# Performance work log

Hardware: AMD Instinct MI355X
Metric: run time of the kernel (lower is better)

The kernel has to match this reference:

```python
import jax, jax.numpy as jnp
import numpy as np

# Fixed hyperparameters from init_kwargs
KH, KW = 3, 3
GRID_SIZE = 5
SPLINE_ORDER = 3
GRID_RANGE = (-1.0, 1.0)


def _make_grid():
    # grid buffer: arange(-k, grid_size + k + 1) * h + grid_range[0], shape (G + 2k + 1,) = (12,)
    h = (GRID_RANGE[1] - GRID_RANGE[0]) / GRID_SIZE
    return (jnp.arange(-SPLINE_ORDER, GRID_SIZE + SPLINE_ORDER + 1, dtype=jnp.float32) * h
            + GRID_RANGE[0])


def _unfold(x):
    # torch.nn.Unfold with kernel (3,3), stride 1, pad 0, dilation 1.
    # Returns (N, C*KH*KW) with channel-major ordering (c, i, j), matching torch.
    B, C, H, W = x.shape
    Ho, Wo = H - KH + 1, W - KW + 1
    cols = [x[:, :, i:i + Ho, j:j + Wo] for i in range(KH) for j in range(KW)]
    p = jnp.stack(cols, axis=2)                    # (B, C, KH*KW, Ho, Wo)
    p = p.reshape(B, C * KH * KW, Ho * Wo)         # (B, in_features, L)
    p = p.transpose(0, 2, 1).reshape(-1, C * KH * KW)  # (B*L, in_features)
    return p, Ho, Wo


def _b_splines(x, grid):
    # x: (N, in_features); grid: (G + 2k + 1,) uniform, shared across features.
    # Returns (N, in_features, G + k) B-spline basis via Cox-de Boor recursion.
    x = x[..., None]  # (N, in, 1)
    bases = ((x >= grid[:-1]) & (x < grid[1:])).astype(x.dtype)  # (N, in, G+2k)
    for k in range(1, SPLINE_ORDER + 1):
        left = (x - grid[: -(k + 1)]) / (grid[k:-1] - grid[: -(k + 1)])
        right = (grid[k + 1:] - x) / (grid[k + 1:] - grid[1:-k])
        bases = left * bases[..., :-1] + right * bases[..., 1:]
    return bases  # (N, in, G + k)


def setup_inputs() -> dict:
    key = jax.random.key(0)
    k1, k2, k3, k4 = jax.random.split(key, 4)
    in_features = 32 * KH * KW  # 288
    out_features = 64
    n_coef = GRID_SIZE + SPLINE_ORDER  # 8
    x = jax.random.normal(k1, (16, 32, 64, 64), dtype=jnp.float32)
    base_weight = jax.random.normal(k2, (out_features, in_features), dtype=jnp.float32) * (1.0 / np.sqrt(in_features))
    spline_weight = jax.random.normal(k3, (out_features, in_features, n_coef), dtype=jnp.float32) * 0.1
    spline_scaler = jax.random.normal(k4, (out_features, in_features), dtype=jnp.float32) * (1.0 / np.sqrt(in_features))
    return {"x": x, "base_weight": base_weight, "spline_weight": spline_weight,
            "spline_scaler": spline_scaler}


def reference(x, base_weight, spline_weight, spline_scaler):
    B = x.shape[0]
    out_features = base_weight.shape[0]
    grid = _make_grid()

    patches, Ho, Wo = _unfold(x)                              # (N, in_features)
    N, in_features = patches.shape

    # KANLinear forward
    base_out = jnp.matmul(jax.nn.relu(patches), base_weight.T)  # (N, out)
    bases = _b_splines(patches, grid)                           # (N, in, G+k)
    scaled_w = spline_weight * spline_scaler[..., None]         # (out, in, G+k)
    spline_out = jnp.matmul(bases.reshape(N, -1), scaled_w.reshape(out_features, -1).T)
    out = base_out + spline_out                                 # (N, out)

    out = out.reshape(B, Ho, Wo, out_features).transpose(0, 3, 1, 2)  # (B, C_out, Ho, Wo)
    return out
```

## Files before the change

### kernel.cpp

```cpp
#include <hip/hip_runtime.h>
#include <stdint.h>

typedef _Float16 half8  __attribute__((ext_vector_type(8)));
typedef float    f32x4  __attribute__((ext_vector_type(4)));
typedef float    f32x16 __attribute__((ext_vector_type(16)));
typedef uint32_t u32x4  __attribute__((ext_vector_type(4)));

#define FIN  288
#define NOUT 64
#define LPB  3844
#define NBF  20736
#define NBAS (16*64*16*64*2)
#define NXR  (16*64*2*64*2)
#define PADS 16

#define SCL  200
#define LDSL (31*SCL + 2*64 + 64 + 8)


__device__ inline half8 bspline8(float xv) {
  float u = fmaf(xv, 2.5f, 5.5f);
  float fi = floorf(u);
  int i = (int)fi;
  float t = u - fi, s = 1.0f - t;
  float t2 = t * t, t3 = t2 * t;
  float s2 = s * s, s3 = s2 * s;
  float w3 = t3 * 0.16666667f;
  float w0 = s3 * 0.16666667f;
  float w1 = fmaf(0.5f, t3, -t2) + 0.66666667f;
  float w2 = fmaf(0.5f, s3, -s2) + 0.66666667f;
  uint32_t u01 = __builtin_bit_cast(uint32_t, __builtin_amdgcn_cvt_pkrtz(w0, w1));
  uint32_t u23 = __builtin_bit_cast(uint32_t, __builtin_amdgcn_cvt_pkrtz(w2, w3));
  uint64_t V = (uint64_t)u01 | ((uint64_t)u23 << 32);
  uint32_t vl = (uint32_t)(V << 16);
  u32x4 fr;
#pragma unroll
  for (int q = 0; q < 4; ++q) {
    int d = i - 2 * q;
    uint32_t rr = (uint32_t)(V >> ((48 - 16 * d) & 63));
    fr[q] = ((uint32_t)d <= 3u) ? rr : ((d == 4) ? vl : 0u);
  }
  return __builtin_bit_cast(half8, fr);
}

__global__ __launch_bounds__(256) void prep_all(const float* __restrict__ x,
                                                const float* __restrict__ bw,
                                                const float* __restrict__ sw,
                                                const float* __restrict__ sc,
                                                half8* __restrict__ ws) {
  int bid = blockIdx.x;
  if (bid < 2048) {
    int t = bid * 256 + threadIdx.x;
    int w4   = t & 15;
    int idx  = t >> 4;
    int half = idx & 1;
    int u    = (idx >> 1) & 15;
    int bh   = idx >> 5;
    int c    = u * 2 + half;
    const float4 v = *(const float4*)(x + (bh >> 6) * 131072 + c * 4096 +
                                      (bh & 63) * 64 + w4 * 4);
    half8* dst = ws + NBF + ((size_t)(bh * 16 + u) * 64 + w4 * 4) * 2 + half;
    dst[0] = bspline8(v.x);
    dst[2] = bspline8(v.y);
    dst[4] = bspline8(v.z);
    dst[6] = bspline8(v.w);
  } else if (bid < 3072) {
    int t = (bid - 2048) * 256 + threadIdx.x;
    int half = t & 1;
    int w    = (t >> 1) & 63;
    int u    = (t >> 7) & 1;
    int bh   = t >> 8;
    const float* xp = x + (bh >> 6) * 131072 + (u * 16 + half * 8) * 4096 +
                      (bh & 63) * 64 + w;
    half8 v;
#pragma unroll
    for (int j = 0; j < 8; ++j) v[j] = (_Float16)fmaxf(xp[j * 4096], 0.0f);
    ws[NBF + NBAS + ((size_t)(bh * 2 + u) * 64 + w) * 2 + half] = v;
  } else {
    int t = (bid - 3072) * 256 + threadIdx.x;
    half8 v;
    int dst;
    if (t < NOUT * FIN) {
      int o = t / FIN;
      int f = t - o * FIN;
      float scale = sc[t];
      const float* p = sw + t * 8;
#pragma unroll
      for (int j = 0; j < 8; ++j) v[j] = (_Float16)(p[j] * scale);
      int c  = f / 9;
      int r  = f - c * 9;
      int ii = r / 3;
      int jj = r - ii * 3;
      int pp = ii * 3 + jj;
      int u  = c >> 1, half = c & 1;
      int nf = o >> 5, col = o & 31;
      dst = pp * 2048 + u * 128 + nf * 64 + half * 32 + col;
    } else {
      int t2 = t - NOUT * FIN;
      int lane = t2 & 63;
      int nf   = (t2 >> 6) & 1;
      int u    = (t2 >> 7) & 1;
      int pos  = t2 >> 8;
      int half = lane >> 5, col = lane & 31;
      int o = nf * 32 + col;
#pragma unroll
      for (int j = 0; j < 8; ++j)
        v[j] = (_Float16)bw[o * FIN + 9 * (u * 16 + half * 8 + j) + pos];
      dst = NOUT * FIN + t2;
    }
    ws[dst] = v;
  }
}

__global__ __launch_bounds__(512, 2) void kan_main(
    const half8* __restrict__ ws,
    float* __restrict__ out) {
  __shared__ __align__(16) unsigned char ldsraw[65536];
  half8* lbf0 = (half8*)ldsraw;
  half8* lbf1 = (half8*)(ldsraw + 32768);
  float* red  = (float*)ldsraw;

  const half8* __restrict__ bfrag = ws;
  const half8* __restrict__ bas   = ws + NBF;
  const half8* __restrict__ xr    = ws + NBF + NBAS;

  const int tid = threadIdx.x;
  int bid0 = blockIdx.x;
  int bid = (bid0 & 7) * 32 + (bid0 >> 3);
  const int b  = bid >> 4;
  const int hg = bid & 15;

  const int lane = tid & 63;
  const int wv   = tid >> 6;
  const int g2   = wv >> 2;
  const int rw   = wv & 3;
  const int l31  = lane & 31;
  const int lhi  = lane >> 5;
  const int laneoff = l31 * 2 + lhi;
  const int ho   = hg * 4 + rw;
  const int hoc  = ho < 61 ? ho : 61;
  const int ulo  = g2 * 8;

  f32x16 acc[2][2];
#pragma unroll
  for (int mt = 0; mt < 2; ++mt)
#pragma unroll
    for (int nf = 0; nf < 2; ++nf)
#pragma unroll
      for (int e = 0; e < 16; ++e) acc[mt][nf][e] = 0.f;

  const half8* bbS = bas + (size_t)(b * 64 + hoc) * 2048 + laneoff;

#pragma unroll
  for (int i = 0; i < 4; ++i) {
    int idx = i * 512 + tid;
    lbf0[idx] = bfrag[idx];
  }
  __syncthreads();
  half8* bcur = lbf0;
  half8* balt = lbf1;

  for (int pp = 0; pp < 9; ++pp) {
    half8 stg[4];
    if (pp < 8) {
      const half8* src = bfrag + (pp + 1) * 2048;
#pragma unroll
      for (int i = 0; i < 4; ++i) stg[i] = src[i * 512 + tid];
    }

    int ii = (pp * 11) >> 5;
    int jj = pp - 3 * ii;
    const half8* pAf = bbS + ii * 2048 + jj * 2;
#pragma unroll
    for (int uu = 0; uu < 8; ++uu) {
      const int u = ulo + uu;
      half8 af0 = pAf[u * 128];
      half8 af1 = pAf[u * 128 + 64];
#pragma unroll
      for (int nf = 0; nf < 2; ++nf) {
        half8 bf = bcur[u * 128 + nf * 64 + lane];
        acc[0][nf] = __builtin_amdgcn_mfma_f32_32x32x16_f16(af0, bf, acc[0][nf], 0, 0, 0);
        acc[1][nf] = __builtin_amdgcn_mfma_f32_32x32x16_f16(af1, bf, acc[1][nf], 0, 0, 0);
      }
    }

    if (pp < 8) {
#pragma unroll
      for (int i = 0; i < 4; ++i) balt[i * 512 + tid] = stg[i];
    }
    __syncthreads();
    half8* t = bcur; bcur = balt; balt = t;
  }

  for (int pos = 0; pos < 9; ++pos) {
    int i2 = (pos * 11) >> 5;
    int j2 = pos - 3 * i2;
    const half8* pAf = xr + (size_t)((b * 64 + hoc + i2) * 2 + g2) * 128 +
                       j2 * 2 + laneoff;
    half8 af0 = pAf[0];
    half8 af1 = pAf[64];
    const half8* bfp = bfrag + NOUT * FIN + (pos * 2 + g2) * 128 + lane;
#pragma unroll
    for (int nf = 0; nf < 2; ++nf) {
      half8 bf = bfp[nf * 64];
      acc[0][nf] = __builtin_amdgcn_mfma_f32_32x32x16_f16(af0, bf, acc[0][nf], 0, 0, 0);
      acc[1][nf] = __builtin_amdgcn_mfma_f32_32x32x16_f16(af1, bf, acc[1][nf], 0, 0, 0);
    }
  }

  if (g2) {
    int base = (rw * 64 + lane) * 64;
#pragma unroll
    for (int mt = 0; mt < 2; ++mt)
#pragma unroll
      for (int nf = 0; nf < 2; ++nf)
#pragma unroll
        for (int q4 = 0; q4 < 4; ++q4) {
          int pos = ((mt * 8 + nf * 4 + q4) + lane) & 15;
          f32x4 ch = {acc[mt][nf][q4 * 4], acc[mt][nf][q4 * 4 + 1],
                      acc[mt][nf][q4 * 4 + 2], acc[mt][nf][q4 * 4 + 3]};
          *(f32x4*)&red[base + pos * 4] = ch;
        }
  }
  __syncthreads();

  if (!g2) {
    int base = (rw * 64 + lane) * 64;
#pragma unroll
    for (int mt = 0; mt < 2; ++mt)
#pragma unroll
      for (int nf = 0; nf < 2; ++nf)
#pragma unroll
        for (int q4 = 0; q4 < 4; ++q4) {
          int pos = ((mt * 8 + nf * 4 + q4) + lane) & 15;
          f32x4 ch = *(const f32x4*)&red[base + pos * 4];
          acc[mt][nf][q4 * 4]     += ch[0];
          acc[mt][nf][q4 * 4 + 1] += ch[1];
          acc[mt][nf][q4 * 4 + 2] += ch[2];
          acc[mt][nf][q4 * 4 + 3] += ch[3];
        }

    if (ho < 62) {
      float* ob = out + b * (NOUT * LPB) + ho * 62;
#pragma unroll
      for (int mt = 0; mt < 2; ++mt) {
#pragma unroll
        for (int reg = 0; reg < 16; ++reg) {
          int wo2 = mt * 32 + (reg & 3) + 8 * (reg >> 2) + 4 * lhi;
          if (wo2 < 62) {
#pragma unroll
            for (int nf = 0; nf < 2; ++nf) {
              int o = nf * 32 + l31;
              ob[o * LPB + wo2] = acc[mt][nf][reg];
            }
          }
        }
      }
    }
  }
}

#define KSPL 72
__global__ void prep_bfrag_legacy(const float* __restrict__ bw,
                                  const float* __restrict__ sw,
                                  const float* __restrict__ sc,
                                  half8* __restrict__ bfrag) {
  int t = blockIdx.x * 256 + threadIdx.x;
  half8 v;
  int dst;
  if (t < NOUT * FIN) {
    int o = t / FIN;
    int f = t - o * FIN;
    float scale = sc[t];
    const float* p = sw + t * 8;
#pragma unroll
    for (int c = 0; c < 8; ++c) v[c] = (_Float16)(p[c] * scale);
    int ch = f / 9;
    int r  = f - ch * 9;
    int ii = r / 3;
    int jj = r - ii * 3;
    int g  = ch >> 2, q = ch & 3;
    int kt = ii * 24 + jj * 8 + g;
    dst = (kt * 4 + (o >> 4)) * 64 + q * 16 + (o & 15);
  } else {
    int t2 = t - NOUT * FIN;
    int lane = t2 & 63;
    int nf = (t2 >> 6) & 3;
    int ktb = t2 >> 8;
    int o = nf * 16 + (lane & 15);
    int f0 = ktb * 32 + (lane >> 4) * 8;
    const float* p = bw + o * FIN + f0;
#pragma unroll
    for (int c = 0; c < 8; ++c) v[c] = (_Float16)p[c];
    dst = ((KSPL + ktb) * 4 + nf) * 64 + lane;
  }
  bfrag[dst] = v;
}

__global__ __launch_bounds__(256, 4) void kan_main_legacy(
    const float* __restrict__ x,
    const half8* __restrict__ bfrag,
    float* __restrict__ out) {
  __shared__ float lx[LDSL];
  const int tid = threadIdx.x;
  const int bid = blockIdx.x;
  const int b  = bid / 62;
  const int ho = bid - b * 62;
  const float* xb = x + b * 131072 + ho * 64;
#pragma unroll
  for (int r = 0; r < 6; ++r) {
    int gid = r * 256 + tid;
    int row = gid >> 4;
    int c   = (row * 683) >> 11;
    int ii  = row - c * 3;
    int colv = (gid & 15) * 4;
    const float4 v = *(const float4*)(xb + c * 4096 + ii * 64 + colv);
    *(float4*)(&lx[c * SCL + ii * 64 + colv]) = v;
  }
  __syncthreads();
  const int lane = tid & 63;
  const int wv   = tid >> 6;
  const int quad = lane >> 4;
  const int m16  = lane & 15;
  const int wo   = wv * 16 + m16;
  f32x4 acc[4];
#pragma unroll
  for (int nf = 0; nf < 4; ++nf) acc[nf] = (f32x4){0.f, 0.f, 0.f, 0.f};
  int kt = 0;
#pragma unroll
  for (int ii = 0; ii < 3; ++ii) {
#pragma unroll
    for (int jj = 0; jj < 3; ++jj) {
      const float* lbase = lx + quad * SCL + ii * 64 + wo + jj;
#pragma unroll
      for (int g = 0; g < 8; ++g) {
        float xv = lbase[g * (4 * SCL)];
        half8 af = bspline8(xv);
#pragma unroll
        for (int nf = 0; nf < 4; ++nf) {
          half8 bf = bfrag[(kt * 4 + nf) * 64 + lane];
          acc[nf] = __builtin_amdgcn_mfma_f32_16x16x32_f16(af, bf, acc[nf], 0, 0, 0);
        }
        ++kt;
      }
    }
  }
#pragma unroll
  for (int kb = 0; kb < 9; ++kb) {
    int f0 = kb * 32 + quad * 8;
    half8 a;
#pragma unroll
    for (int j = 0; j < 8; ++j) {
      int f = f0 + j;
      int c = (f * 57) >> 9;
      int r = f - c * 9;
      int i2 = (r * 11) >> 5;
      int j2 = r - i2 * 3;
      a[j] = (_Float16)fmaxf(lx[c * SCL + i2 * 64 + wo + j2], 0.0f);
    }
#pragma unroll
    for (int nf = 0; nf < 4; ++nf) {
      half8 bf = bfrag[((KSPL + kb) * 4 + nf) * 64 + lane];
      acc[nf] = __builtin_amdgcn_mfma_f32_16x16x32_f16(a, bf, acc[nf], 0, 0, 0);
    }
  }
  float* ob = out + b * (NOUT * LPB) + ho * 62;
#pragma unroll
  for (int rg = 0; rg < 4; ++rg) {
    int wo2 = wv * 16 + quad * 4 + rg;
    if (wo2 < 62) {
#pragma unroll
      for (int nf = 0; nf < 4; ++nf) {
        int o = nf * 16 + m16;
        ob[o * LPB + wo2] = acc[nf][rg];
      }
    }
  }
}

extern "C" void kernel_launch(void* const* d_in, const int* in_sizes, int n_in,
                              void* d_out, int out_size, void* d_ws, size_t ws_size,
                              hipStream_t stream) {
  const float* x  = (const float*)d_in[0];
  const float* bw = (const float*)d_in[1];
  const float* sw = (const float*)d_in[2];
  const float* sc = (const float*)d_in[3];
  float* out = (float*)d_out;
  half8* ws = (half8*)d_ws;

  const size_t need = (size_t)(NBF + NBAS + NXR + PADS) * sizeof(half8);
  if (ws_size >= need) {
    prep_all<<<3153, 256, 0, stream>>>(x, bw, sw, sc, ws);
    kan_main<<<256, 512, 0, stream>>>(ws, out);
  } else {
    prep_bfrag_legacy<<<81, 256, 0, stream>>>(bw, sw, sc, ws);
    kan_main_legacy<<<16 * 62, 256, 0, stream>>>(x, ws, out);
  }
}
```

Before: 119.9 us.

## Software-pipeline A-fragment loads and remap prep threads for coalesced writes

The main kernel's spline loop is fully unrolled with two register banks of A fragments: the next position's 16 global A loads are issued before the current position's MFMAs, and the base-path loads are double-buffered across positions. This aims to hide global load latency behind the matrix math. The prep kernel now gives each thread one element instead of four and writes the basis and relu buffers with contiguous per-thread indices, at the cost of more blocks and scalar input loads. The extra 32 half8 registers per thread raise register pressure and may cost occupancy under the 512-thread, 2-block launch bound.

```diff
diff --git a/kernel.cpp b/kernel.cpp
--- a/kernel.cpp
+++ b/kernel.cpp
@@ -49,35 +49,29 @@
                                                 const float* __restrict__ sc,
                                                 half8* __restrict__ ws) {
   int bid = blockIdx.x;
-  if (bid < 2048) {
+  if (bid < 8192) {
     int t = bid * 256 + threadIdx.x;
-    int w4   = t & 15;
-    int idx  = t >> 4;
-    int half = idx & 1;
-    int u    = (idx >> 1) & 15;
-    int bh   = idx >> 5;
-    int c    = u * 2 + half;
-    const float4 v = *(const float4*)(x + (bh >> 6) * 131072 + c * 4096 +
-                                      (bh & 63) * 64 + w4 * 4);
-    half8* dst = ws + NBF + ((size_t)(bh * 16 + u) * 64 + w4 * 4) * 2 + half;
-    dst[0] = bspline8(v.x);
-    dst[2] = bspline8(v.y);
-    dst[4] = bspline8(v.z);
-    dst[6] = bspline8(v.w);
-  } else if (bid < 3072) {
-    int t = (bid - 2048) * 256 + threadIdx.x;
+    int half = t & 1;
+    int w    = (t >> 1) & 63;
+    int u    = (t >> 7) & 15;
+    int bh   = t >> 11;
+    float xv = x[(size_t)(bh >> 6) * 131072 + (u * 2 + half) * 4096 +
+                 (bh & 63) * 64 + w];
+    ws[NBF + t] = bspline8(xv);
+  } else if (bid < 9216) {
+    int t = (bid - 8192) * 256 + threadIdx.x;
     int half = t & 1;
     int w    = (t >> 1) & 63;
     int u    = (t >> 7) & 1;
     int bh   = t >> 8;
-    const float* xp = x + (bh >> 6) * 131072 + (u * 16 + half * 8) * 4096 +
+    const float* xp = x + (size_t)(bh >> 6) * 131072 + (u * 16 + half * 8) * 4096 +
                       (bh & 63) * 64 + w;
     half8 v;
 #pragma unroll
     for (int j = 0; j < 8; ++j) v[j] = (_Float16)fmaxf(xp[j * 4096], 0.0f);
-    ws[NBF + NBAS + ((size_t)(bh * 2 + u) * 64 + w) * 2 + half] = v;
+    ws[NBF + NBAS + t] = v;
   } else {
-    int t = (bid - 3072) * 256 + threadIdx.x;
+    int t = (bid - 9216) * 256 + threadIdx.x;
     half8 v;
     int dst;
     if (t < NOUT * FIN) {
@@ -112,6 +106,65 @@
   }
 }
 
+#define MFMA32(A, B, C) __builtin_amdgcn_mfma_f32_32x32x16_f16((A), (B), (C), 0, 0, 0)
+
+#define LOAD_AF(PP, AF)                                                     \
+  {                                                                         \
+    const half8* pAf_ = bbS + ((PP) / 3) * 2048 + ((PP) % 3) * 2;           \
+    _Pragma("unroll")                                                       \
+    for (int uu = 0; uu < 8; ++uu) {                                        \
+      AF[uu * 2]     = pAf_[(ulo + uu) * 128];                              \
+      AF[uu * 2 + 1] = pAf_[(ulo + uu) * 128 + 64];                         \
+    }                                                                       \
+  }
+
+#define PAIR(PP, AFC, AFN)                                                  \
+  {                                                                         \
+    half8 stg[4];                                                           \
+    if ((PP) < 8) {                                                         \
+      const half8* src_ = bfrag + ((PP) + 1) * 2048;                        \
+      _Pragma("unroll")                                                     \
+      for (int i = 0; i < 4; ++i) stg[i] = src_[i * 512 + tid];             \
+      LOAD_AF((PP) + 1, AFN)                                                \
+    }                                                                       \
+    _Pragma("unroll")                                                       \
+    for (int uu = 0; uu < 8; ++uu) {                                        \
+      int u_ = ulo + uu;                                                    \
+      _Pragma("unroll")                                                     \
+      for (int nf = 0; nf < 2; ++nf) {                                      \
+        half8 bf_ = bcur[u_ * 128 + nf * 64 + lane];                        \
+        acc[0][nf] = MFMA32(AFC[uu * 2], bf_, acc[0][nf]);                  \
+        acc[1][nf] = MFMA32(AFC[uu * 2 + 1], bf_, acc[1][nf]);              \
+      }                                                                     \
+    }                                                                       \
+    if ((PP) < 8) {                                                         \
+      _Pragma("unroll")                                                     \
+      for (int i = 0; i < 4; ++i) balt[i * 512 + tid] = stg[i];             \
+    }                                                                       \
+    __syncthreads();                                                        \
+    { half8* t_ = bcur; bcur = balt; balt = t_; }                           \
+  }
+
+#define BASE_LOAD(POS, A0, A1, B0, B1)                                      \
+  {                                                                         \
+    constexpr int i2_ = (POS) / 3, j2_ = (POS) - 3 * ((POS) / 3);           \
+    const half8* pAf_ = xr + (size_t)((b * 64 + hoc + i2_) * 2 + g2) * 128 + \
+                        j2_ * 2 + laneoff;                                  \
+    A0 = pAf_[0];                                                           \
+    A1 = pAf_[64];                                                          \
+    const half8* bfp_ = bfrag + NOUT * FIN + ((POS) * 2 + g2) * 128 + lane; \
+    B0 = bfp_[0];                                                           \
+    B1 = bfp_[64];                                                          \
+  }
+
+#define BASE_MMA(A0, A1, B0, B1)                                            \
+  {                                                                         \
+    acc[0][0] = MFMA32(A0, B0, acc[0][0]);                                  \
+    acc[1][0] = MFMA32(A1, B0, acc[1][0]);                                  \
+    acc[0][1] = MFMA32(A0, B1, acc[0][1]);                                  \
+    acc[1][1] = MFMA32(A1, B1, acc[1][1]);                                  \
+  }
+
 __global__ __launch_bounds__(512, 2) void kan_main(
     const half8* __restrict__ ws,
     float* __restrict__ out) {
@@ -151,62 +204,49 @@
 
   const half8* bbS = bas + (size_t)(b * 64 + hoc) * 2048 + laneoff;
 
+  half8 afA[16], afB[16];
+
 #pragma unroll
   for (int i = 0; i < 4; ++i) {
     int idx = i * 512 + tid;
     lbf0[idx] = bfrag[idx];
   }
+  LOAD_AF(0, afA)
   __syncthreads();
   half8* bcur = lbf0;
   half8* balt = lbf1;
 
-  for (int pp = 0; pp < 9; ++pp) {
-    half8 stg[4];
-    if (pp < 8) {
-      const half8* src = bfrag + (pp + 1) * 2048;
-#pragma unroll
-      for (int i = 0; i < 4; ++i) stg[i] = src[i * 512 + tid];
-    }
-
-    int ii = (pp * 11) >> 5;
-    int jj = pp - 3 * ii;
-    const half8* pAf = bbS + ii * 2048 + jj * 2;
-#pragma unroll
-    for (int uu = 0; uu < 8; ++uu) {
-      const int u = ulo + uu;
-      half8 af0 = pAf[u * 128];
-      half8 af1 = pAf[u * 128 + 64];
-#pragma unroll
-      for (int nf = 0; nf < 2; ++nf) {
-        half8 bf = bcur[u * 128 + nf * 64 + lane];
-        acc[0][nf] = __builtin_amdgcn_mfma_f32_32x32x16_f16(af0, bf, acc[0][nf], 0, 0, 0);
-        acc[1][nf] = __builtin_amdgcn_mfma_f32_32x32x16_f16(af1, bf, acc[1][nf], 0, 0, 0);
-      }
-    }
-
-    if (pp < 8) {
-#pragma unroll
-      for (int i = 0; i < 4; ++i) balt[i * 512 + tid] = stg[i];
-    }
-    __syncthreads();
-    half8* t = bcur; bcur = balt; balt = t;
-  }
-
-  for (int pos = 0; pos < 9; ++pos) {
-    int i2 = (pos * 11) >> 5;
-    int j2 = pos - 3 * i2;
-    const half8* pAf = xr + (size_t)((b * 64 + hoc + i2) * 2 + g2) * 128 +
-                       j2 * 2 + laneoff;
-    half8 af0 = pAf[0];
-    half8 af1 = pAf[64];
-    const half8* bfp = bfrag + NOUT * FIN + (pos * 2 + g2) * 128 + lane;
-#pragma unroll
-    for (int nf = 0; nf < 2; ++nf) {
-      half8 bf = bfp[nf * 64];
-      acc[0][nf] = __builtin_amdgcn_mfma_f32_32x32x16_f16(af0, bf, acc[0][nf], 0, 0, 0);
-      acc[1][nf] = __builtin_amdgcn_mfma_f32_32x32x16_f16(af1, bf, acc[1][nf], 0, 0, 0);
-    }
-  }
+  half8 bx0, bx1, bxb0, bxb1;
+  half8 by0, by1, byb0, byb1;
+
+  PAIR(0, afA, afB)
+  PAIR(1, afB, afA)
+  PAIR(2, afA, afB)
+  PAIR(3, afB, afA)
+  PAIR(4, afA, afB)
+  PAIR(5, afB, afA)
+  PAIR(6, afA, afB)
+  PAIR(7, afB, afA)
+  BASE_LOAD(0, bx0, bx1, bxb0, bxb1)
+  PAIR(8, afA, afB)
+
+  BASE_LOAD(1, by0, by1, byb0, byb1)
+  BASE_MMA(bx0, bx1, bxb0, bxb1)
+  BASE_LOAD(2, bx0, bx1, bxb0, bxb1)
+  BASE_MMA(by0, by1, byb0, byb1)
+  BASE_LOAD(3, by0, by1, byb0, byb1)
+  BASE_MMA(bx0, bx1, bxb0, bxb1)
+  BASE_LOAD(4, bx0, bx1, bxb0, bxb1)
+  BASE_MMA(by0, by1, byb0, byb1)
+  BASE_LOAD(5, by0, by1, byb0, byb1)
+  BASE_MMA(bx0, bx1, bxb0, bxb1)
+  BASE_LOAD(6, bx0, bx1, bxb0, bxb1)
+  BASE_MMA(by0, by1, byb0, byb1)
+  BASE_LOAD(7, by0, by1, byb0, byb1)
+  BASE_MMA(bx0, bx1, bxb0, bxb1)
+  BASE_LOAD(8, bx0, bx1, bxb0, bxb1)
+  BASE_MMA(by0, by1, byb0, byb1)
+  BASE_MMA(bx0, bx1, bxb0, bxb1)
 
   if (g2) {
     int base = (rw * 64 + lane) * 64;
@@ -390,7 +430,7 @@
 
   const size_t need = (size_t)(NBF + NBAS + NXR + PADS) * sizeof(half8);
   if (ws_size >= need) {
-    prep_all<<<3153, 256, 0, stream>>>(x, bw, sw, sc, ws);
+    prep_all<<<9297, 256, 0, stream>>>(x, bw, sw, sc, ws);
     kan_main<<<256, 512, 0, stream>>>(ws, out);
   } else {
     prep_bfrag_legacy<<<81, 256, 0, stream>>>(bw, sw, sc, ws);
```

After: 117.5 us. 1.02x faster.
